# Optimization experiments

Hardware: AMD Instinct MI355X
Metric: run time of the kernel (lower is better)

Reference implementation:

```python
import jax, jax.numpy as jnp
import numpy as np

B, S, HID = 2, 2048, 2048
NH, NKV, HD = 32, 8, 64
N_REP = NH // NKV
SCALING = HD ** -0.5
NEG_INF = -1e9


def rotate_half(x):
    x1, x2 = x[..., : x.shape[-1] // 2], x[..., x.shape[-1] // 2 :]
    return jnp.concatenate((-x2, x1), axis=-1)


def setup_inputs() -> dict:
    key = jax.random.key(0)
    ks = jax.random.split(key, 5)
    hidden_states = jax.random.normal(ks[0], (B, S, HID), dtype=jnp.float32)
    # real RoPE tables, theta=10000
    inv_freq = 1.0 / (10000.0 ** (jnp.arange(0, HD, 2, dtype=jnp.float32) / HD))
    freqs = jnp.arange(S, dtype=jnp.float32)[:, None] * inv_freq[None, :]  # [S, HD/2]
    emb = jnp.concatenate((freqs, freqs), axis=-1)  # [S, HD]
    cos = jnp.broadcast_to(jnp.cos(emb)[None], (B, S, HD))
    sin = jnp.broadcast_to(jnp.sin(emb)[None], (B, S, HD))
    # additive causal mask [B, 1, S, S]
    causal = jnp.tril(jnp.ones((S, S), dtype=bool))
    attention_mask = jnp.where(causal, 0.0, NEG_INF).astype(jnp.float32)
    attention_mask = jnp.broadcast_to(attention_mask[None, None], (B, 1, S, S))
    std = 0.02
    Wq = jax.random.normal(ks[1], (NH * HD, HID), dtype=jnp.float32) * std
    Wk = jax.random.normal(ks[2], (NKV * HD, HID), dtype=jnp.float32) * std
    Wv = jax.random.normal(ks[3], (NKV * HD, HID), dtype=jnp.float32) * std
    Wo = jax.random.normal(ks[4], (HID, NH * HD), dtype=jnp.float32) * std
    return {"hidden_states": hidden_states, "cos": cos, "sin": sin,
            "attention_mask": attention_mask, "Wq": Wq, "Wk": Wk, "Wv": Wv, "Wo": Wo}


def reference(hidden_states, cos, sin, attention_mask, Wq, Wk, Wv, Wo):
    b, s, _ = hidden_states.shape
    # projections (nn.Linear: y = x @ W.T), split heads -> [b, h, s, d]
    q = jnp.einsum("bsh,oh->bso", hidden_states, Wq).reshape(b, s, NH, HD).transpose(0, 2, 1, 3)
    k = jnp.einsum("bsh,oh->bso", hidden_states, Wk).reshape(b, s, NKV, HD).transpose(0, 2, 1, 3)
    v = jnp.einsum("bsh,oh->bso", hidden_states, Wv).reshape(b, s, NKV, HD).transpose(0, 2, 1, 3)
    # RoPE (cos/sin unsqueezed at dim 1)
    c, sn = cos[:, None], sin[:, None]
    q = q * c + rotate_half(q) * sn
    k = k * c + rotate_half(k) * sn
    # GQA repeat_kv
    k = jnp.repeat(k, N_REP, axis=1)
    v = jnp.repeat(v, N_REP, axis=1)
    # eager attention: QK^T -> +mask -> fp32 softmax -> V
    logits = jnp.einsum("bhqd,bhkd->bhqk", q, k) * SCALING + attention_mask
    attn_weights = jax.nn.softmax(logits.astype(jnp.float32), axis=-1).astype(q.dtype)
    attn_out = jnp.einsum("bhqk,bhkd->bhqd", attn_weights, v)
    attn_out = attn_out.transpose(0, 2, 1, 3).reshape(b, s, NH * HD)
    out = jnp.einsum("bso,ho->bsh", attn_out, Wo)
    return out, attn_weights
```

## Files before the change

### kernel.cpp

```cpp
#include <hip/hip_runtime.h>
#include <hip/hip_bf16.h>


typedef __bf16 bf16;
typedef bf16 bf16x8 __attribute__((ext_vector_type(8)));
typedef bf16 bf16x4 __attribute__((ext_vector_type(4)));
typedef float f32x4 __attribute__((ext_vector_type(4)));

#define B_   2
#define S_   2048
#define HID_ 2048
#define NH_  32
#define NKV_ 8
#define HD_  64
#define TOK_ (B_*S_)
#define QKVN 3072

__device__ __forceinline__ void gl_lds16(const bf16* g, bf16* l) {
  __builtin_amdgcn_global_load_lds(
      (const __attribute__((address_space(1))) unsigned int*)(g),
      (__attribute__((address_space(3))) unsigned int*)(l), 16, 0, 0);
}

__global__ __launch_bounds__(256) void cast_f32_bf16(const float* __restrict__ in,
                                                     bf16* __restrict__ out, int n4) {
  int i = blockIdx.x * 256 + threadIdx.x;
  if (i >= n4) return;
  f32x4 v = ((const f32x4*)in)[i];
  bf16x4 o;
  o[0] = (bf16)v[0]; o[1] = (bf16)v[1]; o[2] = (bf16)v[2]; o[3] = (bf16)v[3];
  ((bf16x4*)out)[i] = o;
}

__global__ __launch_bounds__(256) void cast_wqkv(const float* __restrict__ wq,
                                                 const float* __restrict__ wk,
                                                 const float* __restrict__ wv,
                                                 bf16* __restrict__ dst) {
  int i = blockIdx.x * 256 + threadIdx.x;
  const float* src; int off;
  if (i < 1048576)      { src = wq; off = i; }
  else if (i < 1310720) { src = wk; off = i - 1048576; }
  else                  { src = wv; off = i - 1310720; }
  f32x4 v = ((const f32x4*)src)[off];
  bf16x4 o;
  o[0] = (bf16)v[0]; o[1] = (bf16)v[1]; o[2] = (bf16)v[2]; o[3] = (bf16)v[3];
  ((bf16x4*)dst)[i] = o;
}

template<bool OUT_F32>
__global__ __launch_bounds__(256) void gemm_bt(const bf16* __restrict__ A,
                                               const bf16* __restrict__ Bm,
                                               void* __restrict__ Cout,
                                               int M, int N, int K) {
  __shared__ __align__(16) bf16 As[128 * 32];
  __shared__ __align__(16) bf16 Bs[128 * 32];
  const int tid  = threadIdx.x;
  const int wave = tid >> 6, lane = tid & 63;

  const int nwg = (int)(gridDim.x * gridDim.y);
  const int bid = (int)(blockIdx.y * gridDim.x + blockIdx.x);
  const int swz = (bid & 7) * (nwg >> 3) + (bid >> 3);
  const int bx = swz % (int)gridDim.x, by = swz / (int)gridDim.x;

  const int bm = by * 128, bn = bx * 128;
  const int wm = (wave >> 1) * 64, wn = (wave & 1) * 64;
  const int fr = lane & 15, fg = lane >> 4;

  const int r0   = wave * 32 + (lane >> 2);
  const int scol = (lane & 3) * 8;
  const bf16* ga0 = A  + (size_t)(bm + r0) * K + scol;
  const bf16* ga1 = ga0 + (size_t)16 * K;
  const bf16* gb0 = Bm + (size_t)(bn + r0) * K + scol;
  const bf16* gb1 = gb0 + (size_t)16 * K;
  bf16* lA0 = As + (wave * 32) * 32;
  bf16* lA1 = lA0 + 16 * 32;
  bf16* lB0 = Bs + (wave * 32) * 32;
  bf16* lB1 = lB0 + 16 * 32;

  f32x4 acc[4][4] = {};

  for (int k0 = 0; k0 < K; k0 += 32) {
    gl_lds16(ga0 + k0, lA0);
    gl_lds16(ga1 + k0, lA1);
    gl_lds16(gb0 + k0, lB0);
    gl_lds16(gb1 + k0, lB1);
    __syncthreads();
    bf16x8 af[4], bfv[4];
#pragma unroll
    for (int i = 0; i < 4; ++i) {
      af[i]  = *(const bf16x8*)&As[(wm + i * 16 + fr) * 32 + fg * 8];
      bfv[i] = *(const bf16x8*)&Bs[(wn + i * 16 + fr) * 32 + fg * 8];
    }
#pragma unroll
    for (int i = 0; i < 4; ++i)
#pragma unroll
      for (int j = 0; j < 4; ++j)
        acc[i][j] = __builtin_amdgcn_mfma_f32_16x16x32_bf16(af[i], bfv[j], acc[i][j], 0, 0, 0);
    __syncthreads();
  }

#pragma unroll
  for (int i = 0; i < 4; ++i)
#pragma unroll
    for (int j = 0; j < 4; ++j)
#pragma unroll
      for (int r = 0; r < 4; ++r) {
        int row = bm + wm + i * 16 + fg * 4 + r;
        int col = bn + wn + j * 16 + fr;
        float v = acc[i][j][r];
        if (OUT_F32) __builtin_nontemporal_store(v, &((float*)Cout)[(size_t)row * N + col]);
        else         ((bf16*)Cout)[(size_t)row * N + col] = (bf16)v;
      }
}

__global__ __launch_bounds__(256) void rope_fused(bf16* __restrict__ qkv,
                                                  const float* __restrict__ cosp,
                                                  const float* __restrict__ sinp) {
  const int t = blockIdx.x;
  const int tid = threadIdx.x;
  const int d = tid & 31, g = tid >> 5;
  const float c = cosp[t * 64 + d];
  const float s = sinp[t * 64 + d];
  bf16* row = qkv + (size_t)t * QKVN;
#pragma unroll
  for (int i = 0; i < 4; ++i) {
    bf16* p = row + (g + i * 8) * 64 + d;
    float x1 = (float)p[0], x2 = (float)p[32];
    p[0]  = (bf16)(x1 * c - x2 * s);
    p[32] = (bf16)(x2 * c + x1 * s);
  }
  bf16* p = row + 2048 + g * 64 + d;
  float x1 = (float)p[0], x2 = (float)p[32];
  p[0]  = (bf16)(x1 * c - x2 * s);
  p[32] = (bf16)(x2 * c + x1 * s);
}

__global__ __launch_bounds__(256) void transpose_v(const bf16* __restrict__ v,
                                                   bf16* __restrict__ vT) {
  __shared__ __align__(16) bf16 t[64][72];
  const int bkv = blockIdx.y;
  const int b = bkv >> 3, kv = bkv & 7;
  const int s0 = blockIdx.x * 64;
  const int tid = threadIdx.x;
  const int r = tid >> 3, c = (tid & 7) * 8;
#pragma unroll
  for (int p = 0; p < 2; ++p) {
    int rr = r + p * 32;
    *(bf16x8*)&t[rr][c] = *(const bf16x8*)&v[(size_t)(b * S_ + s0 + rr) * QKVN + kv * 64 + c];
  }
  __syncthreads();
#pragma unroll
  for (int p = 0; p < 2; ++p) {
    int d = r + p * 32;
    bf16x8 o;
#pragma unroll
    for (int j = 0; j < 8; ++j) o[j] = t[c + j][d];
    *(bf16x8*)&vT[((size_t)bkv * 64 + d) * S_ + s0 + c] = o;
  }
}

__global__ __launch_bounds__(512) void attn_kernel(const bf16* __restrict__ qkv,
                                                   const bf16* __restrict__ vT,
                                                   float* __restrict__ attnw,
                                                   bf16* __restrict__ attn_out)
{
  __shared__ __align__(16) bf16 Ks[64][72];
  __shared__ __align__(16) bf16 Vs[64][72];
  __shared__ __align__(16) bf16 Ps[8][16][72];

  const int tid  = threadIdx.x;
  const int wave = tid >> 6, lane = tid & 63;
  const int qt = (int)gridDim.x - 1 - (int)blockIdx.x;
  const int bh = blockIdx.y;
  const int b = bh >> 5, h = bh & 31, kv = h >> 2;
  const int q0 = qt * 128;
  const int fr = lane & 15, fg = lane >> 4;
  const int row_w = wave * 16;
  const int row_t = row_w + fg * 4;
  const int NT = 2 * qt + 2;

  bf16x8 aq[2];
  {
    const bf16* qp = qkv + (size_t)(b * S_ + q0 + row_w + fr) * QKVN + h * 64 + fg * 8;
    aq[0] = *(const bf16x8*)qp;
    aq[1] = *(const bf16x8*)(qp + 32);
  }

  const int lr = tid >> 3;
  const int lc = (tid & 7) * 8;
  const bf16* kbase = qkv + (size_t)(b * S_) * QKVN + 2048 + kv * 64;
  const bf16* vbase = vT + (size_t)(b * NKV_ + kv) * 64 * S_;

  float rs[4] = {0.f, 0.f, 0.f, 0.f};
  for (int jt = 0; jt < NT; ++jt) {
    const int j0 = jt * 64;
    __syncthreads();
    *(bf16x8*)&Ks[lr][lc] = *(const bf16x8*)&kbase[(size_t)(j0 + lr) * QKVN + lc];
    __syncthreads();
    const bool fullmask = (j0 > q0 + row_w + 15);
    if (fullmask) continue;
    f32x4 acc[4] = {};
#pragma unroll
    for (int nn = 0; nn < 4; ++nn) {
      bf16x8 bk0 = *(const bf16x8*)&Ks[nn*16 + fr][fg*8];
      bf16x8 bk1 = *(const bf16x8*)&Ks[nn*16 + fr][32 + fg*8];
      acc[nn] = __builtin_amdgcn_mfma_f32_16x16x32_bf16(aq[0], bk0, acc[nn], 0, 0, 0);
      acc[nn] = __builtin_amdgcn_mfma_f32_16x16x32_bf16(aq[1], bk1, acc[nn], 0, 0, 0);
    }
    if (j0 + 63 <= q0 + row_w) {
#pragma unroll
      for (int nn = 0; nn < 4; ++nn)
#pragma unroll
        for (int r = 0; r < 4; ++r) rs[r] += __expf(acc[nn][r] * 0.125f);
    } else {
#pragma unroll
      for (int nn = 0; nn < 4; ++nn)
#pragma unroll
        for (int r = 0; r < 4; ++r)
          if (j0 + nn * 16 + fr <= q0 + row_t + r) rs[r] += __expf(acc[nn][r] * 0.125f);
    }
  }
#pragma unroll
  for (int r = 0; r < 4; ++r) {
    float v = rs[r];
    v += __shfl_xor(v, 1); v += __shfl_xor(v, 2);
    v += __shfl_xor(v, 4); v += __shfl_xor(v, 8);
    rs[r] = 1.0f / v;
  }

  f32x4 oacc[4] = {};
  {
    float* awp = attnw + ((size_t)bh * S_ + q0 + row_t) * S_ + fr;
    for (int jt = 0; jt < NT; ++jt) {
      const int j0 = jt * 64;
      __syncthreads();
      *(bf16x8*)&Ks[lr][lc] = *(const bf16x8*)&kbase[(size_t)(j0 + lr) * QKVN + lc];
      *(bf16x8*)&Vs[lr][lc] = *(const bf16x8*)&vbase[(size_t)lr * S_ + j0 + lc];
      __syncthreads();
      const bool fullmask = (j0 > q0 + row_w + 15);
      if (fullmask) {
        f32x4 z = {0.f, 0.f, 0.f, 0.f};
        (void)z;
#pragma unroll
        for (int nn = 0; nn < 4; ++nn)
#pragma unroll
          for (int r = 0; r < 4; ++r)
            __builtin_nontemporal_store(0.f, awp + (size_t)r * S_ + nn * 16);
        awp += 64;
        continue;
      }
      f32x4 acc[4] = {};
#pragma unroll
      for (int nn = 0; nn < 4; ++nn) {
        bf16x8 bk0 = *(const bf16x8*)&Ks[nn*16 + fr][fg*8];
        bf16x8 bk1 = *(const bf16x8*)&Ks[nn*16 + fr][32 + fg*8];
        acc[nn] = __builtin_amdgcn_mfma_f32_16x16x32_bf16(aq[0], bk0, acc[nn], 0, 0, 0);
        acc[nn] = __builtin_amdgcn_mfma_f32_16x16x32_bf16(aq[1], bk1, acc[nn], 0, 0, 0);
      }
      if (j0 + 63 <= q0 + row_w) {
#pragma unroll
        for (int nn = 0; nn < 4; ++nn)
#pragma unroll
          for (int r = 0; r < 4; ++r) {
            float pv = __expf(acc[nn][r] * 0.125f) * rs[r];
            __builtin_nontemporal_store(pv, awp + (size_t)r * S_ + nn * 16);
            Ps[wave][fg * 4 + r][nn * 16 + fr] = (bf16)pv;
          }
      } else {
#pragma unroll
        for (int nn = 0; nn < 4; ++nn)
#pragma unroll
          for (int r = 0; r < 4; ++r) {
            float pv = (j0 + nn * 16 + fr > q0 + row_t + r) ? 0.f
                       : __expf(acc[nn][r] * 0.125f) * rs[r];
            __builtin_nontemporal_store(pv, awp + (size_t)r * S_ + nn * 16);
            Ps[wave][fg * 4 + r][nn * 16 + fr] = (bf16)pv;
          }
      }
      bf16x8 pa0 = *(const bf16x8*)&Ps[wave][fr][fg * 8];
      bf16x8 pa1 = *(const bf16x8*)&Ps[wave][fr][32 + fg * 8];
#pragma unroll
      for (int nn = 0; nn < 4; ++nn) {
        bf16x8 bv0 = *(const bf16x8*)&Vs[nn*16 + fr][fg*8];
        bf16x8 bv1 = *(const bf16x8*)&Vs[nn*16 + fr][32 + fg*8];
        oacc[nn] = __builtin_amdgcn_mfma_f32_16x16x32_bf16(pa0, bv0, oacc[nn], 0, 0, 0);
        oacc[nn] = __builtin_amdgcn_mfma_f32_16x16x32_bf16(pa1, bv1, oacc[nn], 0, 0, 0);
      }
      awp += 64;
    }
  }

#pragma unroll
  for (int nn = 0; nn < 4; ++nn)
#pragma unroll
    for (int r = 0; r < 4; ++r) {
      int row = q0 + row_t + r;
      attn_out[(size_t)(b * S_ + row) * (NH_*HD_) + h * 64 + nn * 16 + fr] = (bf16)oacc[nn][r];
    }

  const int zc0 = NT * 64;
  f32x4 z4 = {0.f, 0.f, 0.f, 0.f};
  for (int rr = 0; rr < 16; ++rr) {
    size_t base = ((size_t)bh * S_ + q0 + row_w + rr) * S_;
    for (int c = zc0 + lane * 4; c < S_; c += 256)
      __builtin_nontemporal_store(z4, (f32x4*)&attnw[base + c]);
  }
}

extern "C" void kernel_launch(void* const* d_in, const int* in_sizes, int n_in,
                              void* d_out, int out_size, void* d_ws, size_t ws_size,
                              hipStream_t stream) {
  const float* hs   = (const float*)d_in[0];
  const float* cosp = (const float*)d_in[1];
  const float* sinp = (const float*)d_in[2];
  const float* Wq = (const float*)d_in[4];
  const float* Wk = (const float*)d_in[5];
  const float* Wv = (const float*)d_in[6];
  const float* Wo = (const float*)d_in[7];

  char* ws = (char*)d_ws;
  bf16* hs_b   = (bf16*)(ws);
  bf16* qkv_b  = (bf16*)(ws + (16u << 20));
  bf16* vT_b   = (bf16*)(ws + (40u << 20));
  bf16* ao_b   = (bf16*)(ws + (44u << 20));
  bf16* Wqkv_b = (bf16*)(ws + (60u << 20));
  bf16* Wo_b   = (bf16*)(ws + (72u << 20));

  float* outp  = (float*)d_out;
  float* attnw = outp + (size_t)TOK_ * HID_;

  cast_f32_bf16<<<(TOK_*HID_/4 + 255)/256, 256, 0, stream>>>(hs, hs_b, TOK_*HID_/4);
  cast_wqkv<<<(1572864 + 255)/256, 256, 0, stream>>>(Wq, Wk, Wv, Wqkv_b);
  cast_f32_bf16<<<(HID_*NH_*HD_/4 + 255)/256, 256, 0, stream>>>(Wo, Wo_b, HID_*NH_*HD_/4);

  gemm_bt<false><<<dim3(QKVN/128, TOK_/128), 256, 0, stream>>>(hs_b, Wqkv_b, qkv_b, TOK_, QKVN, HID_);

  rope_fused<<<TOK_, 256, 0, stream>>>(qkv_b, cosp, sinp);

  transpose_v<<<dim3(S_/64, B_*NKV_), 256, 0, stream>>>(qkv_b + 2560, vT_b);

  attn_kernel<<<dim3(S_/128, B_*NH_), 512, 0, stream>>>(qkv_b, vT_b, attnw, ao_b);

  gemm_bt<true><<<dim3(HID_/128, TOK_/128), 256, 0, stream>>>(ao_b, Wo_b, outp, TOK_, HID_, HID_);
}
```

Before: 526.1 us.

## Pair low and high causal query tiles per block with register-prefetched K/V

Each block now handles two 64-row query tiles, one near the start and one near the end of the sequence, so every block does the same amount of causal work. K and V tiles are staged once and shared by both tiles. The block size drops to 256 threads with an occupancy hint, and the next K/V tile is prefetched into registers while the current one is used. The zero-fill of the masked region is moved ahead of the main PV loop. In exchange the kernel holds more registers (two Q sets and two accumulators), which could lower occupancy.

After: 494.5 us. 1.06x faster.

```diff
diff --git a/kernel.cpp b/kernel.cpp
--- a/kernel.cpp
+++ b/kernel.cpp
@@ -159,134 +159,233 @@
   }
 }
 
-__global__ __launch_bounds__(512) void attn_kernel(const bf16* __restrict__ qkv,
-                                                   const bf16* __restrict__ vT,
-                                                   float* __restrict__ attnw,
-                                                   bf16* __restrict__ attn_out)
+__global__ __launch_bounds__(256, 4) void attn_kernel(const bf16* __restrict__ qkv,
+                                                      const bf16* __restrict__ vT,
+                                                      float* __restrict__ attnw,
+                                                      bf16* __restrict__ attn_out)
 {
   __shared__ __align__(16) bf16 Ks[64][72];
   __shared__ __align__(16) bf16 Vs[64][72];
-  __shared__ __align__(16) bf16 Ps[8][16][72];
+  __shared__ __align__(16) bf16 Ps[4][16][72];
 
   const int tid  = threadIdx.x;
   const int wave = tid >> 6, lane = tid & 63;
-  const int qt = (int)gridDim.x - 1 - (int)blockIdx.x;
+  const int qt = blockIdx.x;
   const int bh = blockIdx.y;
   const int b = bh >> 5, h = bh & 31, kv = h >> 2;
-  const int q0 = qt * 128;
+  const int qLo = qt * 64;
+  const int qHi = (31 - qt) * 64;
+  const int NT  = 32 - qt;
   const int fr = lane & 15, fg = lane >> 4;
-  const int row_w = wave * 16;
-  const int row_t = row_w + fg * 4;
-  const int NT = 2 * qt + 2;
-
-  bf16x8 aq[2];
+  const int rw = wave * 16;
+  const int rt = rw + fg * 4;
+
+  bf16x8 aqL[2], aqH[2];
   {
-    const bf16* qp = qkv + (size_t)(b * S_ + q0 + row_w + fr) * QKVN + h * 64 + fg * 8;
-    aq[0] = *(const bf16x8*)qp;
-    aq[1] = *(const bf16x8*)(qp + 32);
-  }
-
-  const int lr = tid >> 3;
-  const int lc = (tid & 7) * 8;
+    const bf16* qp = qkv + (size_t)(b * S_ + qLo + rw + fr) * QKVN + h * 64 + fg * 8;
+    aqL[0] = *(const bf16x8*)qp;  aqL[1] = *(const bf16x8*)(qp + 32);
+    qp = qkv + (size_t)(b * S_ + qHi + rw + fr) * QKVN + h * 64 + fg * 8;
+    aqH[0] = *(const bf16x8*)qp;  aqH[1] = *(const bf16x8*)(qp + 32);
+  }
+
+  const int lr = tid >> 2;
+  const int lc = (tid & 3) * 16;
   const bf16* kbase = qkv + (size_t)(b * S_) * QKVN + 2048 + kv * 64;
   const bf16* vbase = vT + (size_t)(b * NKV_ + kv) * 64 * S_;
-
-  float rs[4] = {0.f, 0.f, 0.f, 0.f};
-  for (int jt = 0; jt < NT; ++jt) {
-    const int j0 = jt * 64;
-    __syncthreads();
-    *(bf16x8*)&Ks[lr][lc] = *(const bf16x8*)&kbase[(size_t)(j0 + lr) * QKVN + lc];
-    __syncthreads();
-    const bool fullmask = (j0 > q0 + row_w + 15);
-    if (fullmask) continue;
-    f32x4 acc[4] = {};
-#pragma unroll
-    for (int nn = 0; nn < 4; ++nn) {
-      bf16x8 bk0 = *(const bf16x8*)&Ks[nn*16 + fr][fg*8];
-      bf16x8 bk1 = *(const bf16x8*)&Ks[nn*16 + fr][32 + fg*8];
-      acc[nn] = __builtin_amdgcn_mfma_f32_16x16x32_bf16(aq[0], bk0, acc[nn], 0, 0, 0);
-      acc[nn] = __builtin_amdgcn_mfma_f32_16x16x32_bf16(aq[1], bk1, acc[nn], 0, 0, 0);
-    }
-    if (j0 + 63 <= q0 + row_w) {
-#pragma unroll
-      for (int nn = 0; nn < 4; ++nn)
-#pragma unroll
-        for (int r = 0; r < 4; ++r) rs[r] += __expf(acc[nn][r] * 0.125f);
-    } else {
-#pragma unroll
-      for (int nn = 0; nn < 4; ++nn)
-#pragma unroll
-        for (int r = 0; r < 4; ++r)
-          if (j0 + nn * 16 + fr <= q0 + row_t + r) rs[r] += __expf(acc[nn][r] * 0.125f);
+  const bf16* kst = kbase + (size_t)lr * QKVN + lc;
+  const bf16* vst = vbase + (size_t)lr * S_ + lc;
+
+  float rsL[4] = {0.f,0.f,0.f,0.f}, rsH[4] = {0.f,0.f,0.f,0.f};
+  {
+    bf16x8 kr0 = *(const bf16x8*)(kst);
+    bf16x8 kr1 = *(const bf16x8*)(kst + 8);
+    for (int jt = 0; jt < NT; ++jt) {
+      __syncthreads();
+      *(bf16x8*)&Ks[lr][lc]     = kr0;
+      *(bf16x8*)&Ks[lr][lc + 8] = kr1;
+      __syncthreads();
+      if (jt + 1 < NT) {
+        const bf16* p = kst + (size_t)(jt + 1) * 64 * QKVN;
+        kr0 = *(const bf16x8*)(p);
+        kr1 = *(const bf16x8*)(p + 8);
+      }
+      {
+        f32x4 acc[4] = {};
+#pragma unroll
+        for (int nn = 0; nn < 4; ++nn) {
+          bf16x8 bk0 = *(const bf16x8*)&Ks[nn*16 + fr][fg*8];
+          bf16x8 bk1 = *(const bf16x8*)&Ks[nn*16 + fr][32 + fg*8];
+          acc[nn] = __builtin_amdgcn_mfma_f32_16x16x32_bf16(aqH[0], bk0, acc[nn], 0, 0, 0);
+          acc[nn] = __builtin_amdgcn_mfma_f32_16x16x32_bf16(aqH[1], bk1, acc[nn], 0, 0, 0);
+        }
+        if (jt < NT - 1) {
+#pragma unroll
+          for (int nn = 0; nn < 4; ++nn)
+#pragma unroll
+            for (int r = 0; r < 4; ++r) rsH[r] += __expf(acc[nn][r] * 0.125f);
+        } else {
+#pragma unroll
+          for (int nn = 0; nn < 4; ++nn)
+#pragma unroll
+            for (int r = 0; r < 4; ++r)
+              if (nn * 16 + fr <= rt + r) rsH[r] += __expf(acc[nn][r] * 0.125f);
+        }
+      }
+      if (jt <= qt) {
+        f32x4 acc[4] = {};
+#pragma unroll
+        for (int nn = 0; nn < 4; ++nn) {
+          bf16x8 bk0 = *(const bf16x8*)&Ks[nn*16 + fr][fg*8];
+          bf16x8 bk1 = *(const bf16x8*)&Ks[nn*16 + fr][32 + fg*8];
+          acc[nn] = __builtin_amdgcn_mfma_f32_16x16x32_bf16(aqL[0], bk0, acc[nn], 0, 0, 0);
+          acc[nn] = __builtin_amdgcn_mfma_f32_16x16x32_bf16(aqL[1], bk1, acc[nn], 0, 0, 0);
+        }
+        if (jt < qt) {
+#pragma unroll
+          for (int nn = 0; nn < 4; ++nn)
+#pragma unroll
+            for (int r = 0; r < 4; ++r) rsL[r] += __expf(acc[nn][r] * 0.125f);
+        } else {
+#pragma unroll
+          for (int nn = 0; nn < 4; ++nn)
+#pragma unroll
+            for (int r = 0; r < 4; ++r)
+              if (nn * 16 + fr <= rt + r) rsL[r] += __expf(acc[nn][r] * 0.125f);
+        }
+      }
     }
   }
 #pragma unroll
   for (int r = 0; r < 4; ++r) {
-    float v = rs[r];
+    float v = rsL[r];
     v += __shfl_xor(v, 1); v += __shfl_xor(v, 2);
     v += __shfl_xor(v, 4); v += __shfl_xor(v, 8);
-    rs[r] = 1.0f / v;
-  }
-
-  f32x4 oacc[4] = {};
+    rsL[r] = 1.0f / v;
+    v = rsH[r];
+    v += __shfl_xor(v, 1); v += __shfl_xor(v, 2);
+    v += __shfl_xor(v, 4); v += __shfl_xor(v, 8);
+    rsH[r] = 1.0f / v;
+  }
+
   {
-    float* awp = attnw + ((size_t)bh * S_ + q0 + row_t) * S_ + fr;
+    f32x4 z4 = {0.f, 0.f, 0.f, 0.f};
+    const int zLo = (qt + 1) * 64;
+    for (int rr = 0; rr < 16; ++rr) {
+      size_t base = ((size_t)bh * S_ + qLo + rw + rr) * S_;
+      for (int c = zLo + lane * 4; c < S_; c += 256)
+        __builtin_nontemporal_store(z4, (f32x4*)&attnw[base + c]);
+    }
+    const int zHi = NT * 64;
+    for (int rr = 0; rr < 16; ++rr) {
+      size_t base = ((size_t)bh * S_ + qHi + rw + rr) * S_;
+      for (int c = zHi + lane * 4; c < S_; c += 256)
+        __builtin_nontemporal_store(z4, (f32x4*)&attnw[base + c]);
+    }
+  }
+
+  f32x4 oL[4] = {}, oH[4] = {};
+  {
+    float* awpL = attnw + ((size_t)bh * S_ + qLo + rt) * S_ + fr;
+    float* awpH = attnw + ((size_t)bh * S_ + qHi + rt) * S_ + fr;
+    bf16x8 kr0 = *(const bf16x8*)(kst);
+    bf16x8 kr1 = *(const bf16x8*)(kst + 8);
+    bf16x8 vr0 = *(const bf16x8*)(vst);
+    bf16x8 vr1 = *(const bf16x8*)(vst + 8);
     for (int jt = 0; jt < NT; ++jt) {
-      const int j0 = jt * 64;
       __syncthreads();
-      *(bf16x8*)&Ks[lr][lc] = *(const bf16x8*)&kbase[(size_t)(j0 + lr) * QKVN + lc];
-      *(bf16x8*)&Vs[lr][lc] = *(const bf16x8*)&vbase[(size_t)lr * S_ + j0 + lc];
+      *(bf16x8*)&Ks[lr][lc]     = kr0;
+      *(bf16x8*)&Ks[lr][lc + 8] = kr1;
+      *(bf16x8*)&Vs[lr][lc]     = vr0;
+      *(bf16x8*)&Vs[lr][lc + 8] = vr1;
       __syncthreads();
-      const bool fullmask = (j0 > q0 + row_w + 15);
-      if (fullmask) {
-        f32x4 z = {0.f, 0.f, 0.f, 0.f};
-        (void)z;
-#pragma unroll
-        for (int nn = 0; nn < 4; ++nn)
-#pragma unroll
-          for (int r = 0; r < 4; ++r)
-            __builtin_nontemporal_store(0.f, awp + (size_t)r * S_ + nn * 16);
-        awp += 64;
-        continue;
-      }
-      f32x4 acc[4] = {};
-#pragma unroll
-      for (int nn = 0; nn < 4; ++nn) {
-        bf16x8 bk0 = *(const bf16x8*)&Ks[nn*16 + fr][fg*8];
-        bf16x8 bk1 = *(const bf16x8*)&Ks[nn*16 + fr][32 + fg*8];
-        acc[nn] = __builtin_amdgcn_mfma_f32_16x16x32_bf16(aq[0], bk0, acc[nn], 0, 0, 0);
-        acc[nn] = __builtin_amdgcn_mfma_f32_16x16x32_bf16(aq[1], bk1, acc[nn], 0, 0, 0);
-      }
-      if (j0 + 63 <= q0 + row_w) {
-#pragma unroll
-        for (int nn = 0; nn < 4; ++nn)
-#pragma unroll
-          for (int r = 0; r < 4; ++r) {
-            float pv = __expf(acc[nn][r] * 0.125f) * rs[r];
-            __builtin_nontemporal_store(pv, awp + (size_t)r * S_ + nn * 16);
-            Ps[wave][fg * 4 + r][nn * 16 + fr] = (bf16)pv;
-          }
-      } else {
-#pragma unroll
-        for (int nn = 0; nn < 4; ++nn)
-#pragma unroll
-          for (int r = 0; r < 4; ++r) {
-            float pv = (j0 + nn * 16 + fr > q0 + row_t + r) ? 0.f
-                       : __expf(acc[nn][r] * 0.125f) * rs[r];
-            __builtin_nontemporal_store(pv, awp + (size_t)r * S_ + nn * 16);
-            Ps[wave][fg * 4 + r][nn * 16 + fr] = (bf16)pv;
-          }
-      }
-      bf16x8 pa0 = *(const bf16x8*)&Ps[wave][fr][fg * 8];
-      bf16x8 pa1 = *(const bf16x8*)&Ps[wave][fr][32 + fg * 8];
-#pragma unroll
-      for (int nn = 0; nn < 4; ++nn) {
-        bf16x8 bv0 = *(const bf16x8*)&Vs[nn*16 + fr][fg*8];
-        bf16x8 bv1 = *(const bf16x8*)&Vs[nn*16 + fr][32 + fg*8];
-        oacc[nn] = __builtin_amdgcn_mfma_f32_16x16x32_bf16(pa0, bv0, oacc[nn], 0, 0, 0);
-        oacc[nn] = __builtin_amdgcn_mfma_f32_16x16x32_bf16(pa1, bv1, oacc[nn], 0, 0, 0);
-      }
-      awp += 64;
+      if (jt + 1 < NT) {
+        const bf16* p = kst + (size_t)(jt + 1) * 64 * QKVN;
+        kr0 = *(const bf16x8*)(p);
+        kr1 = *(const bf16x8*)(p + 8);
+        p = vst + (size_t)(jt + 1) * 64;
+        vr0 = *(const bf16x8*)(p);
+        vr1 = *(const bf16x8*)(p + 8);
+      }
+      {
+        f32x4 acc[4] = {};
+#pragma unroll
+        for (int nn = 0; nn < 4; ++nn) {
+          bf16x8 bk0 = *(const bf16x8*)&Ks[nn*16 + fr][fg*8];
+          bf16x8 bk1 = *(const bf16x8*)&Ks[nn*16 + fr][32 + fg*8];
+          acc[nn] = __builtin_amdgcn_mfma_f32_16x16x32_bf16(aqH[0], bk0, acc[nn], 0, 0, 0);
+          acc[nn] = __builtin_amdgcn_mfma_f32_16x16x32_bf16(aqH[1], bk1, acc[nn], 0, 0, 0);
+        }
+        if (jt < NT - 1) {
+#pragma unroll
+          for (int nn = 0; nn < 4; ++nn)
+#pragma unroll
+            for (int r = 0; r < 4; ++r) {
+              float pv = __expf(acc[nn][r] * 0.125f) * rsH[r];
+              __builtin_nontemporal_store(pv, awpH + (size_t)r * S_ + nn * 16);
+              Ps[wave][fg * 4 + r][nn * 16 + fr] = (bf16)pv;
+            }
+        } else {
+#pragma unroll
+          for (int nn = 0; nn < 4; ++nn)
+#pragma unroll
+            for (int r = 0; r < 4; ++r) {
+              float pv = (nn * 16 + fr > rt + r) ? 0.f
+                         : __expf(acc[nn][r] * 0.125f) * rsH[r];
+              __builtin_nontemporal_store(pv, awpH + (size_t)r * S_ + nn * 16);
+              Ps[wave][fg * 4 + r][nn * 16 + fr] = (bf16)pv;
+            }
+        }
+        bf16x8 pa0 = *(const bf16x8*)&Ps[wave][fr][fg * 8];
+        bf16x8 pa1 = *(const bf16x8*)&Ps[wave][fr][32 + fg * 8];
+#pragma unroll
+        for (int nn = 0; nn < 4; ++nn) {
+          bf16x8 bv0 = *(const bf16x8*)&Vs[nn*16 + fr][fg*8];
+          bf16x8 bv1 = *(const bf16x8*)&Vs[nn*16 + fr][32 + fg*8];
+          oH[nn] = __builtin_amdgcn_mfma_f32_16x16x32_bf16(pa0, bv0, oH[nn], 0, 0, 0);
+          oH[nn] = __builtin_amdgcn_mfma_f32_16x16x32_bf16(pa1, bv1, oH[nn], 0, 0, 0);
+        }
+        awpH += 64;
+      }
+      if (jt <= qt) {
+        f32x4 acc[4] = {};
+#pragma unroll
+        for (int nn = 0; nn < 4; ++nn) {
+          bf16x8 bk0 = *(const bf16x8*)&Ks[nn*16 + fr][fg*8];
+          bf16x8 bk1 = *(const bf16x8*)&Ks[nn*16 + fr][32 + fg*8];
+          acc[nn] = __builtin_amdgcn_mfma_f32_16x16x32_bf16(aqL[0], bk0, acc[nn], 0, 0, 0);
+          acc[nn] = __builtin_amdgcn_mfma_f32_16x16x32_bf16(aqL[1], bk1, acc[nn], 0, 0, 0);
+        }
+        if (jt < qt) {
+#pragma unroll
+          for (int nn = 0; nn < 4; ++nn)
+#pragma unroll
+            for (int r = 0; r < 4; ++r) {
+              float pv = __expf(acc[nn][r] * 0.125f) * rsL[r];
+              __builtin_nontemporal_store(pv, awpL + (size_t)r * S_ + nn * 16);
+              Ps[wave][fg * 4 + r][nn * 16 + fr] = (bf16)pv;
+            }
+        } else {
+#pragma unroll
+          for (int nn = 0; nn < 4; ++nn)
+#pragma unroll
+            for (int r = 0; r < 4; ++r) {
+              float pv = (nn * 16 + fr > rt + r) ? 0.f
+                         : __expf(acc[nn][r] * 0.125f) * rsL[r];
+              __builtin_nontemporal_store(pv, awpL + (size_t)r * S_ + nn * 16);
+              Ps[wave][fg * 4 + r][nn * 16 + fr] = (bf16)pv;
+            }
+        }
+        bf16x8 pa0 = *(const bf16x8*)&Ps[wave][fr][fg * 8];
+        bf16x8 pa1 = *(const bf16x8*)&Ps[wave][fr][32 + fg * 8];
+#pragma unroll
+        for (int nn = 0; nn < 4; ++nn) {
+          bf16x8 bv0 = *(const bf16x8*)&Vs[nn*16 + fr][fg*8];
+          bf16x8 bv1 = *(const bf16x8*)&Vs[nn*16 + fr][32 + fg*8];
+          oL[nn] = __builtin_amdgcn_mfma_f32_16x16x32_bf16(pa0, bv0, oL[nn], 0, 0, 0);
+          oL[nn] = __builtin_amdgcn_mfma_f32_16x16x32_bf16(pa1, bv1, oL[nn], 0, 0, 0);
+        }
+        awpL += 64;
+      }
     }
   }
 
@@ -294,17 +393,11 @@
   for (int nn = 0; nn < 4; ++nn)
 #pragma unroll
     for (int r = 0; r < 4; ++r) {
-      int row = q0 + row_t + r;
-      attn_out[(size_t)(b * S_ + row) * (NH_*HD_) + h * 64 + nn * 16 + fr] = (bf16)oacc[nn][r];
-    }
-
-  const int zc0 = NT * 64;
-  f32x4 z4 = {0.f, 0.f, 0.f, 0.f};
-  for (int rr = 0; rr < 16; ++rr) {
-    size_t base = ((size_t)bh * S_ + q0 + row_w + rr) * S_;
-    for (int c = zc0 + lane * 4; c < S_; c += 256)
-      __builtin_nontemporal_store(z4, (f32x4*)&attnw[base + c]);
-  }
+      int rowL = qLo + rt + r;
+      int rowH = qHi + rt + r;
+      attn_out[(size_t)(b * S_ + rowL) * (NH_*HD_) + h * 64 + nn * 16 + fr] = (bf16)oL[nn][r];
+      attn_out[(size_t)(b * S_ + rowH) * (NH_*HD_) + h * 64 + nn * 16 + fr] = (bf16)oH[nn][r];
+    }
 }
 
 extern "C" void kernel_launch(void* const* d_in, const int* in_sizes, int n_in,
@@ -339,7 +432,7 @@
 
   transpose_v<<<dim3(S_/64, B_*NKV_), 256, 0, stream>>>(qkv_b + 2560, vT_b);
 
-  attn_kernel<<<dim3(S_/128, B_*NH_), 512, 0, stream>>>(qkv_b, vT_b, attnw, ao_b);
+  attn_kernel<<<dim3(S_/128, B_*NH_), 256, 0, stream>>>(qkv_b, vT_b, attnw, ao_b);
 
   gemm_bt<true><<<dim3(HID_/128, TOK_/128), 256, 0, stream>>>(ao_b, Wo_b, outp, TOK_, HID_, HID_);
 }
```
